# Kernel optimization log

Hardware: AMD Instinct MI355X
Metric: run time of the kernel (lower is better)

The kernel has to match this reference:

```python
import jax, jax.numpy as jnp
import numpy as np

BN_EPS = 1e-5
MAX_NODES = 35  # sigmoid()*30+5 floored -> in [5, 34], strict bound 35


def _bn_eval(x, gamma, beta, rm, rv):
    # BatchNorm1d in eval mode with running statistics
    return (x - rm) * (gamma / jnp.sqrt(rv + BN_EPS)) + beta


def setup_inputs() -> dict:
    key = jax.random.key(0)
    ks = jax.random.split(key, 32)
    B, LD, E, ND = 131072, 32, 64, 11

    def lin(k, fan_in, fan_out):
        k1, k2 = jax.random.split(k)
        lim = 1.0 / np.sqrt(fan_in)
        w = jax.random.uniform(k1, (fan_in, fan_out), jnp.float32, -lim, lim)
        b = jax.random.uniform(k2, (fan_out,), jnp.float32, -lim, lim)
        return w, b

    lin_w, lin_b = lin(ks[0], LD + 1, E)
    nn1_w, nn1_b = lin(ks[1], E, E)
    nn2_w, nn2_b = lin(ks[2], E, 1)
    nd1_w, nd1_b = lin(ks[3], E, E)
    nd2_w, nd2_b = lin(ks[4], E, ND)
    pd1_w, pd1_b = lin(ks[5], E, E)
    pd2_w, pd2_b = lin(ks[6], E, 3)

    def bn_params(k):
        k1, k2, k3, k4 = jax.random.split(k, 4)
        gamma = 1.0 + 0.1 * jax.random.normal(k1, (E,), jnp.float32)
        beta = 0.1 * jax.random.normal(k2, (E,), jnp.float32)
        rm = 0.1 * jax.random.normal(k3, (E,), jnp.float32)
        rv = jax.random.uniform(k4, (E,), jnp.float32, 0.5, 1.5)
        return gamma, beta, rm, rv

    nd_gamma, nd_beta, nd_rm, nd_rv = bn_params(ks[7])
    pd_gamma, pd_beta, pd_rm, pd_rv = bn_params(ks[8])

    return dict(
        z=jax.random.normal(ks[9], (B, LD), jnp.float32),
        target_property=jax.random.normal(ks[10], (B,), jnp.float32),
        batch_size=B,
        lin_w=lin_w, lin_b=lin_b,
        nn1_w=nn1_w, nn1_b=nn1_b, nn2_w=nn2_w, nn2_b=nn2_b,
        nd1_w=nd1_w, nd1_b=nd1_b, nd_gamma=nd_gamma, nd_beta=nd_beta,
        nd_rm=nd_rm, nd_rv=nd_rv, nd2_w=nd2_w, nd2_b=nd2_b,
        pd1_w=pd1_w, pd1_b=pd1_b, pd_gamma=pd_gamma, pd_beta=pd_beta,
        pd_rm=pd_rm, pd_rv=pd_rv, pd2_w=pd2_w, pd2_b=pd2_b,
        node_scale=jnp.float32(4.5), node_shift=jnp.float32(4.5),
        pos_scale=jnp.float32(5.0), pos_shift=jnp.float32(0.0),
    )


def reference(z, target_property, batch_size,
              lin_w, lin_b,
              nn1_w, nn1_b, nn2_w, nn2_b,
              nd1_w, nd1_b, nd_gamma, nd_beta, nd_rm, nd_rv, nd2_w, nd2_b,
              pd1_w, pd1_b, pd_gamma, pd_beta, pd_rm, pd_rv, pd2_w, pd2_b,
              node_scale, node_shift, pos_scale, pos_shift):
    tp = target_property.reshape(-1, 1)
    h = jnp.concatenate([z, tp], axis=1) @ lin_w + lin_b  # [B, E]

    nn_logit = jax.nn.relu(h @ nn1_w + nn1_b) @ nn2_w + nn2_b  # [B, 1]
    num_nodes = (jax.nn.sigmoid(nn_logit) * 30.0 + 5.0).astype(jnp.int32)[:, 0]  # [B]

    # Expanded rows per graph are identical copies of h[i], so decode once per
    # graph (BN in eval mode) and repeat -> same math as per-graph expand+MLP.
    nf = _bn_eval(jax.nn.relu(h @ nd1_w + nd1_b), nd_gamma, nd_beta, nd_rm, nd_rv) @ nd2_w + nd2_b
    nf = nf * node_scale + node_shift  # [B, 11]
    pos = _bn_eval(jax.nn.relu(h @ pd1_w + pd1_b), pd_gamma, pd_beta, pd_rm, pd_rv) @ pd2_w + pd2_b
    pos = pos * pos_scale + pos_shift  # [B, 3]

    total = batch_size * MAX_NODES  # static padded bound on ragged concat length
    node_features = jnp.repeat(nf, num_nodes, axis=0, total_repeat_length=total)
    positions = jnp.repeat(pos, num_nodes, axis=0, total_repeat_length=total)
    return node_features, positions, num_nodes
```

## Files before the change

### kernel.cpp

```cpp
#include <hip/hip_runtime.h>
#include <math.h>

typedef unsigned int u32;
typedef unsigned short u16;
typedef unsigned char u8;
typedef __attribute__((ext_vector_type(8))) short short8v;
typedef __attribute__((ext_vector_type(4))) float f32x4;

#define NDF 11
#define MAXN 35
#define RS 72

__device__ __forceinline__ u16 f2bf(float x) {
    u32 b = __float_as_uint(x);
    u32 r = (b + 0x7fffu + ((b >> 16) & 1u)) >> 16;
    return (u16)r;
}
__device__ __forceinline__ float bf2f(u16 h) {
    return __uint_as_float(((u32)h) << 16);
}
__device__ __forceinline__ void splitbf(float x, u16& hi, u16& lo) {
    hi = f2bf(x);
    lo = f2bf(x - bf2f(hi));
}

__global__ void k_prep(const float* __restrict__ lin_w,
                       const float* __restrict__ nn1_w, const float* __restrict__ nn2_w,
                       const float* __restrict__ nd1_w, const float* __restrict__ nd2_w,
                       const float* __restrict__ pd1_w, const float* __restrict__ pd2_w,
                       const float* __restrict__ nd_g, const float* __restrict__ nd_be,
                       const float* __restrict__ nd_rm, const float* __restrict__ nd_rv,
                       const float* __restrict__ pd_g, const float* __restrict__ pd_be,
                       const float* __restrict__ pd_rm, const float* __restrict__ pd_rv,
                       u16* __restrict__ lint, u16* __restrict__ w1t3,
                       u16* __restrict__ w2t3, float* __restrict__ bnc)
{
    const int t0 = blockIdx.x * 256 + threadIdx.x;
    if (t0 < 64) {
        const float sc = nd_g[t0] / sqrtf(nd_rv[t0] + 1e-5f);
        bnc[t0]       = sc;
        bnc[64 + t0]  = nd_be[t0] - nd_rm[t0] * sc;
        const float sp = pd_g[t0] / sqrtf(pd_rv[t0] + 1e-5f);
        bnc[128 + t0] = sp;
        bnc[192 + t0] = pd_be[t0] - pd_rm[t0] * sp;
    }
    for (int i = t0; i < 64*RS; i += 4096) {
        const int n = i / RS, k = i % RS;
        const float v = (k < 33) ? lin_w[k*64 + n] : 0.f;
        u16 h, l; splitbf(v, h, l);
        lint[i] = h; lint[64*RS + i] = l;
    }
    for (int b = 0; b < 3; b++) {
        const float* M = (b == 0) ? nn1_w : (b == 1) ? nd1_w : pd1_w;
        u16* dst = w1t3 + (size_t)b * 2 * 64 * RS;
        for (int i = t0; i < 64*RS; i += 4096) {
            const int o = i / RS, k = i % RS;
            const float v = (k < 64) ? M[k*64 + o] : 0.f;
            u16 h, l; splitbf(v, h, l);
            dst[i] = h; dst[64*RS + i] = l;
        }
        u16* d2 = w2t3 + (size_t)b * 2 * 16 * RS;
        for (int i = t0; i < 16*RS; i += 4096) {
            const int n = i / RS, k = i % RS;
            float v = 0.f;
            if (k < 64) {
                if (b == 0)      { if (n == 14)           v = nn2_w[k]; }
                else if (b == 1) { if (n < 11)            v = nd2_w[k*11 + n]; }
                else             { if (n >= 11 && n < 14) v = pd2_w[k*3 + (n-11)]; }
            }
            u16 h, l; splitbf(v, h, l);
            d2[i] = h; d2[16*RS + i] = l;
        }
    }
}

__global__ __launch_bounds__(256)
void k_mfma(const float* __restrict__ z, const float* __restrict__ tpr,
            const float* __restrict__ lin_b,
            const u16* __restrict__ lint, const u16* __restrict__ w1t3,
            const u16* __restrict__ w2t3,
            const float* __restrict__ nn1_b, const float* __restrict__ nd1_b,
            const float* __restrict__ pd1_b,
            const float* __restrict__ nn2_b, const float* __restrict__ nd2_b,
            const float* __restrict__ pd2_b,
            const float* __restrict__ bnc,
            const float* __restrict__ nsc, const float* __restrict__ nsh,
            const float* __restrict__ psc, const float* __restrict__ psh,
            float* __restrict__ nf_g, float* __restrict__ pos_g,
            int* __restrict__ nn_int, float* __restrict__ out_nn,
            u8* __restrict__ flag, int B)
{
    __shared__ __align__(16) u16 sXT[4][2*16*RS];
    __shared__ __align__(16) u16 sH[4][2*16*RS];

    const int t    = threadIdx.x;
    const int lane = t & 63;
    const int w    = t >> 6;
    u16* mX = sXT[w];
    u16* mH = sH[w];

    const int W = blockIdx.x * 4 + w;

    auto zeroXpad = [&]() {
        if (lane < 16) {
            #pragma unroll
            for (int pl = 0; pl < 2; pl++) {
                u16* base = mX + pl*16*RS;
                base[lane*RS + 33] = 0;
                u32* p = (u32*)(base + lane*RS + 34);
                #pragma unroll
                for (int q = 0; q < 15; q++) p[q] = 0;
            }
        }
    };

    auto gfrag = [&](const u16* base, int row0, int ks) -> short8v {
        const uint4 v = *(const uint4*)(base + (row0 + (lane & 15))*RS + ks*32 + ((lane >> 4) * 8));
        return __builtin_bit_cast(short8v, v);
    };
    short8v fLin[4][2], fW[3][4][2], fH2[3][2];
    #pragma unroll
    for (int nt = 0; nt < 4; nt++)
        #pragma unroll
        for (int ks = 0; ks < 2; ks++)
            fLin[nt][ks] = gfrag(lint, nt*16, ks);
    #pragma unroll
    for (int b = 0; b < 3; b++)
        #pragma unroll
        for (int nt = 0; nt < 4; nt++)
            #pragma unroll
            for (int ks = 0; ks < 2; ks++)
                fW[b][nt][ks] = gfrag(w1t3 + (size_t)b*2*64*RS, nt*16, ks);
    #pragma unroll
    for (int b = 0; b < 3; b++)
        #pragma unroll
        for (int ks = 0; ks < 2; ks++)
            fH2[b][ks] = gfrag(w2t3 + (size_t)b*2*16*RS, 0, ks);

    const int col = lane & 15;
    float bLin[4], bB1[3][4], bSc[2][4], bBi[2][4];
    #pragma unroll
    for (int nt = 0; nt < 4; nt++) {
        const int c = nt*16 + col;
        bLin[nt]    = lin_b[c];
        bB1[0][nt]  = nn1_b[c];
        bB1[1][nt]  = nd1_b[c];
        bB1[2][nt]  = pd1_b[c];
        bSc[0][nt]  = bnc[c];        bBi[0][nt] = bnc[64 + c];
        bSc[1][nt]  = bnc[128 + c];  bBi[1][nt] = bnc[192 + c];
    }
    const float epb = (col < 11) ? nd2_b[col] : (col < 14) ? pd2_b[col - 11] : 0.f;
    const float nn2b = nn2_b[0];
    const float a_ns = nsc[0], a_nh = nsh[0], a_ps = psc[0], a_ph = psh[0];

    auto ldfrag = [&](const u16* base, int ks) -> short8v {
        const uint4 v = *(const uint4*)(base + (lane & 15)*RS + ks*32 + ((lane >> 4) * 8));
        return __builtin_bit_cast(short8v, v);
    };

    #pragma unroll 1
    for (int c = 0; c < 2; c++) {
        const int gb = (W*2 + c) * 16;
        if (gb >= B) break;

        zeroXpad();

        {
            const float4* zb = (const float4*)(z + (size_t)gb * 32);
            const float4 v0 = zb[(lane >> 2)*8 + (lane & 3)*2];
            const float4 v1 = zb[(lane >> 2)*8 + (lane & 3)*2 + 1];
            const float xv[8] = {v0.x, v0.y, v0.z, v0.w, v1.x, v1.y, v1.z, v1.w};
            u32 pkh[4], pkl[4];
            #pragma unroll
            for (int q = 0; q < 4; q++) {
                u16 h0, l0, h1, l1;
                splitbf(xv[2*q], h0, l0);
                splitbf(xv[2*q+1], h1, l1);
                pkh[q] = (u32)h0 | ((u32)h1 << 16);
                pkl[q] = (u32)l0 | ((u32)l1 << 16);
            }
            *(uint4*)(mX + (lane >> 2)*RS + (lane & 3)*8) = *(uint4*)pkh;
            *(uint4*)(mX + 16*RS + (lane >> 2)*RS + (lane & 3)*8) = *(uint4*)pkl;
            if (lane < 16) {
                u16 h, l; splitbf(tpr[gb + lane], h, l);
                mX[lane*RS + 32] = h;
                mX[16*RS + lane*RS + 32] = l;
            }
        }

        const short8v a0h = ldfrag(mX, 0);
        const short8v a1h = ldfrag(mX, 1);
        const short8v a0l = ldfrag(mX + 16*RS, 0);
        const short8v a1l = ldfrag(mX + 16*RS, 1);
        #pragma unroll
        for (int nt = 0; nt < 4; nt++) {
            const short8v bl0 = gfrag(lint + 64*RS, nt*16, 0);
            const short8v bl1 = gfrag(lint + 64*RS, nt*16, 1);
            f32x4 acc = {0.f, 0.f, 0.f, 0.f};
            acc = __builtin_amdgcn_mfma_f32_16x16x32_bf16(a0h, fLin[nt][0], acc, 0, 0, 0);
            acc = __builtin_amdgcn_mfma_f32_16x16x32_bf16(a1h, fLin[nt][1], acc, 0, 0, 0);
            acc = __builtin_amdgcn_mfma_f32_16x16x32_bf16(a0h, bl0, acc, 0, 0, 0);
            acc = __builtin_amdgcn_mfma_f32_16x16x32_bf16(a1h, bl1, acc, 0, 0, 0);
            acc = __builtin_amdgcn_mfma_f32_16x16x32_bf16(a0l, fLin[nt][0], acc, 0, 0, 0);
            acc = __builtin_amdgcn_mfma_f32_16x16x32_bf16(a1l, fLin[nt][1], acc, 0, 0, 0);
            const float bias = bLin[nt];
            #pragma unroll
            for (int r = 0; r < 4; r++) {
                const int row = (lane >> 4)*4 + r;
                u16 hh, hl; splitbf(acc[r] + bias, hh, hl);
                mH[row*RS + nt*16 + col] = hh;
                mH[16*RS + row*RS + nt*16 + col] = hl;
            }
        }

        u16* mT = mX;
        const short8v h0h = ldfrag(mH, 0);
        const short8v h1h = ldfrag(mH, 1);
        f32x4 acc2 = {0.f, 0.f, 0.f, 0.f};

        {
            const short8v h0l = ldfrag(mH + 16*RS, 0);
            const short8v h1l = ldfrag(mH + 16*RS, 1);
            const u16* wlo = w1t3 + 64*RS;
            #pragma unroll
            for (int nt = 0; nt < 4; nt++) {
                const short8v wl0 = gfrag(wlo, nt*16, 0);
                const short8v wl1 = gfrag(wlo, nt*16, 1);
                f32x4 acc = {0.f, 0.f, 0.f, 0.f};
                acc = __builtin_amdgcn_mfma_f32_16x16x32_bf16(h0h, fW[0][nt][0], acc, 0, 0, 0);
                acc = __builtin_amdgcn_mfma_f32_16x16x32_bf16(h1h, fW[0][nt][1], acc, 0, 0, 0);
                acc = __builtin_amdgcn_mfma_f32_16x16x32_bf16(h0h, wl0, acc, 0, 0, 0);
                acc = __builtin_amdgcn_mfma_f32_16x16x32_bf16(h1h, wl1, acc, 0, 0, 0);
                acc = __builtin_amdgcn_mfma_f32_16x16x32_bf16(h0l, fW[0][nt][0], acc, 0, 0, 0);
                acc = __builtin_amdgcn_mfma_f32_16x16x32_bf16(h1l, fW[0][nt][1], acc, 0, 0, 0);
                const float bb = bB1[0][nt];
                #pragma unroll
                for (int r = 0; r < 4; r++) {
                    const int row = (lane >> 4)*4 + r;
                    float rv = acc[r] + bb;
                    rv = rv > 0.f ? rv : 0.f;
                    u16 th, tl; splitbf(rv, th, tl);
                    mT[row*RS + nt*16 + col] = th;
                    mT[16*RS + row*RS + nt*16 + col] = tl;
                }
            }
            const short8v t0h = ldfrag(mT, 0);
            const short8v t1h = ldfrag(mT, 1);
            const short8v t0l = ldfrag(mT + 16*RS, 0);
            const short8v t1l = ldfrag(mT + 16*RS, 1);
            const short8v g2l0 = gfrag(w2t3 + 16*RS, 0, 0);
            const short8v g2l1 = gfrag(w2t3 + 16*RS, 0, 1);
            acc2 = __builtin_amdgcn_mfma_f32_16x16x32_bf16(t0h, fH2[0][0], acc2, 0, 0, 0);
            acc2 = __builtin_amdgcn_mfma_f32_16x16x32_bf16(t1h, fH2[0][1], acc2, 0, 0, 0);
            acc2 = __builtin_amdgcn_mfma_f32_16x16x32_bf16(t0h, g2l0, acc2, 0, 0, 0);
            acc2 = __builtin_amdgcn_mfma_f32_16x16x32_bf16(t1h, g2l1, acc2, 0, 0, 0);
            acc2 = __builtin_amdgcn_mfma_f32_16x16x32_bf16(t0l, fH2[0][0], acc2, 0, 0, 0);
            acc2 = __builtin_amdgcn_mfma_f32_16x16x32_bf16(t1l, fH2[0][1], acc2, 0, 0, 0);
        }

        #pragma unroll
        for (int b = 1; b < 3; b++) {
            #pragma unroll
            for (int nt = 0; nt < 4; nt++) {
                f32x4 acc = {0.f, 0.f, 0.f, 0.f};
                acc = __builtin_amdgcn_mfma_f32_16x16x32_bf16(h0h, fW[b][nt][0], acc, 0, 0, 0);
                acc = __builtin_amdgcn_mfma_f32_16x16x32_bf16(h1h, fW[b][nt][1], acc, 0, 0, 0);
                const float bb = bB1[b][nt];
                const float sc = bSc[b-1][nt];
                const float bi = bBi[b-1][nt];
                #pragma unroll
                for (int r = 0; r < 4; r++) {
                    const int row = (lane >> 4)*4 + r;
                    float rv = acc[r] + bb;
                    rv = rv > 0.f ? rv : 0.f;
                    mT[row*RS + nt*16 + col] = f2bf(fmaf(rv, sc, bi));
                }
            }
            const short8v t0 = ldfrag(mT, 0);
            const short8v t1 = ldfrag(mT, 1);
            acc2 = __builtin_amdgcn_mfma_f32_16x16x32_bf16(t0, fH2[b][0], acc2, 0, 0, 0);
            acc2 = __builtin_amdgcn_mfma_f32_16x16x32_bf16(t1, fH2[b][1], acc2, 0, 0, 0);
        }

        #pragma unroll
        for (int r = 0; r < 4; r++) {
            const int g = gb + (lane >> 4)*4 + r;
            const float v = acc2[r];
            if (col < 11) {
                nf_g[(size_t)g*NDF + col] = fmaf(v + epb, a_ns, a_nh);
            } else if (col < 14) {
                pos_g[(size_t)g*3 + (col - 11)] = fmaf(v + epb, a_ps, a_ph);
            } else if (col == 14) {
                const float logit = v + nn2b;
                const float arg = fmaf(1.f / (1.f + expf(-logit)), 30.f, 5.f);
                const int n = (int)arg;
                nn_int[g] = n;
                out_nn[g] = (float)n;
                flag[g] = (fabsf(arg - rintf(arg)) < 0.03f) ? 1 : 0;
            }
        }
    }
    (void)B;
}

__global__ __launch_bounds__(256)
void k_fix(const float* __restrict__ z, const float* __restrict__ tpr,
           const float* __restrict__ lin_w, const float* __restrict__ lin_b,
           const float* __restrict__ nn1_w, const float* __restrict__ nn1_b,
           const float* __restrict__ nn2_w, const float* __restrict__ nn2_b,
           const u8* __restrict__ flag, int* __restrict__ nn_int,
           float* __restrict__ out_nn, int B)
{
    __shared__ __align__(16) double hb[4][64];
    const int lane = threadIdx.x & 63;
    const int w = threadIdx.x >> 6;
    const int W = (blockIdx.x * 256 + threadIdx.x) >> 6;
    const int gpw = B / 4096;
    const int g0 = W * gpw;
    const double b2 = (double)nn2_b[0];

    for (int i = 0; i < gpw; i++) {
        const int g = g0 + i;
        if (!flag[g]) continue;

        double h0 = (double)lin_b[lane], h1 = 0.0, h2 = 0.0, h3 = 0.0;
        for (int j = 0; j < 32; j += 4) {
            h0 = fma((double)z[(size_t)g*32 + j],     (double)lin_w[j*64 + lane],     h0);
            h1 = fma((double)z[(size_t)g*32 + j + 1], (double)lin_w[(j+1)*64 + lane], h1);
            h2 = fma((double)z[(size_t)g*32 + j + 2], (double)lin_w[(j+2)*64 + lane], h2);
            h3 = fma((double)z[(size_t)g*32 + j + 3], (double)lin_w[(j+3)*64 + lane], h3);
        }
        h0 = fma((double)tpr[g], (double)lin_w[32*64 + lane], h0);
        hb[w][lane] = (h0 + h1) + (h2 + h3);

        const double2* hp = (const double2*)hb[w];
        double a0 = (double)nn1_b[lane], a1 = 0.0, a2 = 0.0, a3 = 0.0;
        for (int m = 0; m < 16; m++) {
            const double2 p = hp[2*m];
            const double2 q = hp[2*m + 1];
            a0 = fma(p.x, (double)nn1_w[(4*m+0)*64 + lane], a0);
            a1 = fma(p.y, (double)nn1_w[(4*m+1)*64 + lane], a1);
            a2 = fma(q.x, (double)nn1_w[(4*m+2)*64 + lane], a2);
            a3 = fma(q.y, (double)nn1_w[(4*m+3)*64 + lane], a3);
        }
        const double a = (a0 + a1) + (a2 + a3);
        double v = (a > 0.0) ? a * (double)nn2_w[lane] : 0.0;
        for (int d = 32; d > 0; d >>= 1) v += __shfl_xor(v, d);
        const double logit = v + b2;

        if (lane == 0) {
            const double sg = 1.0 / (1.0 + exp(-logit));
            const int n = (int)(sg * 30.0 + 5.0);
            nn_int[g] = n;
            out_nn[g] = (float)n;
        }
    }
}

__global__ __launch_bounds__(256)
void k_scan1(const int* __restrict__ a, int* __restrict__ part, int* __restrict__ bsum)
{
    const int t = threadIdx.x;
    const int lane = t & 63;
    const int wid = t >> 6;
    const int g = blockIdx.x * 256 + t;
    int v = a[g];
    #pragma unroll
    for (int d = 1; d < 64; d <<= 1) {
        const int u = __shfl_up(v, d);
        if (lane >= d) v += u;
    }
    __shared__ int ws[4];
    if (lane == 63) ws[wid] = v;
    __syncthreads();
    int add = 0;
    #pragma unroll
    for (int q = 0; q < 3; q++) if (q < wid) add += ws[q];
    v += add;
    part[g] = v;
    if (t == 255) bsum[blockIdx.x] = v;
}

__global__ void k_scan2(const int* __restrict__ bsum, int* __restrict__ boff, int nb)
{
    const int t = threadIdx.x;
    const int lane = t & 63;
    const int wid = t >> 6;
    const int orig = bsum[t];
    int v = orig;
    #pragma unroll
    for (int d = 1; d < 64; d <<= 1) {
        const int u = __shfl_up(v, d);
        if (lane >= d) v += u;
    }
    __shared__ int ws[8];
    if (lane == 63) ws[wid] = v;
    __syncthreads();
    int add = 0;
    #pragma unroll
    for (int q = 0; q < 7; q++) if (q < wid) add += ws[q];
    v += add;
    boff[t] = v - orig;
    if (t == nb - 1) boff[nb] = v;
}

__global__ __launch_bounds__(256)
void k_expand(const int* __restrict__ part, const int* __restrict__ boff,
              const float* __restrict__ nf_g, const float* __restrict__ pos_g,
              float* __restrict__ out, int B, int T, int nb)
{
    __shared__ __align__(16) float s_nf[512*NDF];
    __shared__ __align__(16) float s_ps[512*3];
    const int t = threadIdx.x;
    const int r0 = blockIdx.x * 512 + 2*t;

    int blo = 0, bhi = nb - 1;
    while (blo < bhi) {
        const int m = (blo + bhi + 1) >> 1;
        if (boff[m] <= r0) blo = m; else bhi = m - 1;
    }
    const int bi = blo;
    const int lr = r0 - boff[bi];
    int lo = 0, hi2 = 256;
    while (lo < hi2) {
        const int m = (lo + hi2) >> 1;
        if (part[bi*256 + m] <= lr) lo = m + 1; else hi2 = m;
    }
    int i0 = bi*256 + lo;
    i0 = (i0 < B) ? i0 : B - 1;
    const int Ci0 = boff[i0 >> 8] + part[i0];
    const int i1 = ((r0 + 1) >= Ci0 && i0 < B - 1) ? i0 + 1 : i0;

    #pragma unroll
    for (int j = 0; j < NDF; j++) {
        s_nf[(2*t)*NDF + j]     = nf_g[(size_t)i0*NDF + j];
        s_nf[(2*t + 1)*NDF + j] = nf_g[(size_t)i1*NDF + j];
    }
    #pragma unroll
    for (int j = 0; j < 3; j++) {
        s_ps[(2*t)*3 + j]     = pos_g[(size_t)i0*3 + j];
        s_ps[(2*t + 1)*3 + j] = pos_g[(size_t)i1*3 + j];
    }
    __syncthreads();

    float4* onf = (float4*)(out + (size_t)blockIdx.x * 512 * NDF);
    const float4* snf = (const float4*)s_nf;
    #pragma unroll
    for (int q = 0; q < 6; q++) {
        const int idx = q*256 + t;
        if (idx < 512*NDF/4) onf[idx] = snf[idx];
    }
    float4* ops = (float4*)(out + (size_t)T*NDF + (size_t)blockIdx.x * 512 * 3);
    const float4* sps = (const float4*)s_ps;
    #pragma unroll
    for (int q = 0; q < 2; q++) {
        const int idx = q*256 + t;
        if (idx < 384) ops[idx] = sps[idx];
    }
}

extern "C" void kernel_launch(void* const* d_in, const int* in_sizes, int n_in,
                              void* d_out, int out_size, void* d_ws, size_t ws_size,
                              hipStream_t stream)
{
    const float* z     = (const float*)d_in[0];
    const float* tpr   = (const float*)d_in[1];
    const int    B     = in_sizes[1];
    const int    T     = B * MAXN;

    const float* lin_w = (const float*)d_in[3];
    const float* lin_b = (const float*)d_in[4];
    const float* nn1_w = (const float*)d_in[5];
    const float* nn1_b = (const float*)d_in[6];
    const float* nn2_w = (const float*)d_in[7];
    const float* nn2_b = (const float*)d_in[8];
    const float* nd1_w = (const float*)d_in[9];
    const float* nd1_b = (const float*)d_in[10];
    const float* nd_g  = (const float*)d_in[11];
    const float* nd_be = (const float*)d_in[12];
    const float* nd_rm = (const float*)d_in[13];
    const float* nd_rv = (const float*)d_in[14];
    const float* nd2_w = (const float*)d_in[15];
    const float* nd2_b = (const float*)d_in[16];
    const float* pd1_w = (const float*)d_in[17];
    const float* pd1_b = (const float*)d_in[18];
    const float* pd_g  = (const float*)d_in[19];
    const float* pd_be = (const float*)d_in[20];
    const float* pd_rm = (const float*)d_in[21];
    const float* pd_rv = (const float*)d_in[22];
    const float* pd2_w = (const float*)d_in[23];
    const float* pd2_b = (const float*)d_in[24];
    const float* nsc   = (const float*)d_in[25];
    const float* nsh   = (const float*)d_in[26];
    const float* psc   = (const float*)d_in[27];
    const float* psh   = (const float*)d_in[28];

    float* out = (float*)d_out;

    char* wsp = (char*)d_ws;
    size_t off = 0;
    auto take = [&](size_t bytes) { void* p = wsp + off; off = (off + bytes + 255) & ~(size_t)255; return p; };

    u16*   lint  = (u16*)take(2*64*RS*sizeof(u16));
    u16*   w1t3  = (u16*)take(3*2*64*RS*sizeof(u16));
    u16*   w2t3  = (u16*)take(3*2*16*RS*sizeof(u16));
    float* bnc   = (float*)take(256*sizeof(float));
    u8*    flag  = (u8*)take((size_t)B);
    float* nf_g  = (float*)take((size_t)B*NDF*sizeof(float));
    float* pos_g = (float*)take((size_t)B*3*sizeof(float));
    int*   nn_i  = (int*)take((size_t)B*sizeof(int));
    int*   part  = (int*)take((size_t)B*sizeof(int));
    int*   bsum  = (int*)take(4096*sizeof(int));
    int*   boff  = (int*)take(4096*sizeof(int));

    const int nb = B / 256;

    k_prep<<<16, 256, 0, stream>>>(lin_w, nn1_w, nn2_w, nd1_w, nd2_w, pd1_w, pd2_w,
                                   nd_g, nd_be, nd_rm, nd_rv,
                                   pd_g, pd_be, pd_rm, pd_rv,
                                   lint, w1t3, w2t3, bnc);

    k_mfma<<<B/128, 256, 0, stream>>>(z, tpr, lin_b, lint, w1t3, w2t3,
                                      nn1_b, nd1_b, pd1_b, nn2_b, nd2_b, pd2_b,
                                      bnc, nsc, nsh, psc, psh,
                                      nf_g, pos_g, nn_i, out + (size_t)T*14,
                                      flag, B);

    k_fix<<<1024, 256, 0, stream>>>(z, tpr, lin_w, lin_b, nn1_w, nn1_b, nn2_w, nn2_b,
                                    flag, nn_i, out + (size_t)T*14, B);

    k_scan1<<<nb, 256, 0, stream>>>(nn_i, part, bsum);
    k_scan2<<<1, nb, 0, stream>>>(bsum, boff, nb);

    k_expand<<<T/512, 256, 0, stream>>>(part, boff, nf_g, pos_g, out, B, T, nb);

    (void)n_in; (void)out_size; (void)ws_size;
}
```

Baseline: 141.6 us.

## Pack fix-up flags into per-wave bitmasks and cache block offsets in LDS

The MFMA kernel now ballots its near-integer flags into a 32-bit mask per wave instead of writing a byte per graph. The double-precision fix-up kernel iterates only over set bits, so it no longer scans every flag byte. Graphs whose sigmoid output saturates near 5 or 35 are resolved directly, which removes spurious flags at the clamp edges. The expand kernel also stages the block-offset table in shared memory for its binary search, at the cost of an extra sync and a shared-memory fill per block.

```diff
diff --git a/kernel.cpp b/kernel.cpp
--- a/kernel.cpp
+++ b/kernel.cpp
@@ -3,7 +3,6 @@
 
 typedef unsigned int u32;
 typedef unsigned short u16;
-typedef unsigned char u8;
 typedef __attribute__((ext_vector_type(8))) short short8v;
 typedef __attribute__((ext_vector_type(4))) float f32x4;
 
@@ -88,7 +87,7 @@
             const float* __restrict__ psc, const float* __restrict__ psh,
             float* __restrict__ nf_g, float* __restrict__ pos_g,
             int* __restrict__ nn_int, float* __restrict__ out_nn,
-            u8* __restrict__ flag, int B)
+            u32* __restrict__ fmask, int B)
 {
     __shared__ __align__(16) u16 sXT[4][2*16*RS];
     __shared__ __align__(16) u16 sH[4][2*16*RS];
@@ -157,6 +156,8 @@
         const uint4 v = *(const uint4*)(base + (lane & 15)*RS + ks*32 + ((lane >> 4) * 8));
         return __builtin_bit_cast(short8v, v);
     };
+
+    u32 wavebits = 0;
 
     #pragma unroll 1
     for (int c = 0; c < 2; c++) {
@@ -282,10 +283,12 @@
             acc2 = __builtin_amdgcn_mfma_f32_16x16x32_bf16(t1, fH2[b][1], acc2, 0, 0, 0);
         }
 
+        u32 chunkbits = 0;
         #pragma unroll
         for (int r = 0; r < 4; r++) {
             const int g = gb + (lane >> 4)*4 + r;
             const float v = acc2[r];
+            bool fl = false;
             if (col < 11) {
                 nf_g[(size_t)g*NDF + col] = fmaf(v + epb, a_ns, a_nh);
             } else if (col < 14) {
@@ -293,13 +296,29 @@
             } else if (col == 14) {
                 const float logit = v + nn2b;
                 const float arg = fmaf(1.f / (1.f + expf(-logit)), 30.f, 5.f);
-                const int n = (int)arg;
+                int n;
+                if (arg < 5.03f) {
+                    n = 5;
+                } else if (arg >= 34.97f) {
+                    if (logit >= 38.f)      n = 35;
+                    else { n = 34; fl = (logit > 37.f); }
+                } else {
+                    n = (int)arg;
+                    fl = fabsf(arg - rintf(arg)) < 0.03f;
+                }
                 nn_int[g] = n;
                 out_nn[g] = (float)n;
-                flag[g] = (fabsf(arg - rintf(arg)) < 0.03f) ? 1 : 0;
-            }
-        }
-    }
+            }
+            const unsigned long long m = __ballot(fl);
+            chunkbits |= (u32)(((m >> 14) & 1ull) << r)
+                       | (u32)(((m >> 30) & 1ull) << (4 + r))
+                       | (u32)(((m >> 46) & 1ull) << (8 + r))
+                       | (u32)(((m >> 62) & 1ull) << (12 + r));
+        }
+        wavebits |= chunkbits << (16 * c);
+    }
+
+    if (lane == 0) fmask[W] = wavebits;
     (void)B;
 }
 
@@ -308,20 +327,20 @@
            const float* __restrict__ lin_w, const float* __restrict__ lin_b,
            const float* __restrict__ nn1_w, const float* __restrict__ nn1_b,
            const float* __restrict__ nn2_w, const float* __restrict__ nn2_b,
-           const u8* __restrict__ flag, int* __restrict__ nn_int,
+           const u32* __restrict__ fmask, int* __restrict__ nn_int,
            float* __restrict__ out_nn, int B)
 {
     __shared__ __align__(16) double hb[4][64];
     const int lane = threadIdx.x & 63;
     const int w = threadIdx.x >> 6;
     const int W = (blockIdx.x * 256 + threadIdx.x) >> 6;
-    const int gpw = B / 4096;
-    const int g0 = W * gpw;
+    u32 mask = fmask[W];
     const double b2 = (double)nn2_b[0];
 
-    for (int i = 0; i < gpw; i++) {
-        const int g = g0 + i;
-        if (!flag[g]) continue;
+    while (mask) {
+        const int bpos = __ffs(mask) - 1;
+        mask &= mask - 1;
+        const int g = W * 32 + bpos;
 
         double h0 = (double)lin_b[lane], h1 = 0.0, h2 = 0.0, h3 = 0.0;
         for (int j = 0; j < 32; j += 4) {
@@ -355,6 +374,7 @@
             out_nn[g] = (float)n;
         }
     }
+    (void)B;
 }
 
 __global__ __launch_bounds__(256)
@@ -411,16 +431,20 @@
 {
     __shared__ __align__(16) float s_nf[512*NDF];
     __shared__ __align__(16) float s_ps[512*3];
+    __shared__ int s_boff[513];
     const int t = threadIdx.x;
+    for (int i = t; i <= nb; i += 256) s_boff[i] = boff[i];
+    __syncthreads();
+
     const int r0 = blockIdx.x * 512 + 2*t;
 
     int blo = 0, bhi = nb - 1;
     while (blo < bhi) {
         const int m = (blo + bhi + 1) >> 1;
-        if (boff[m] <= r0) blo = m; else bhi = m - 1;
+        if (s_boff[m] <= r0) blo = m; else bhi = m - 1;
     }
     const int bi = blo;
-    const int lr = r0 - boff[bi];
+    const int lr = r0 - s_boff[bi];
     int lo = 0, hi2 = 256;
     while (lo < hi2) {
         const int m = (lo + hi2) >> 1;
@@ -428,7 +452,7 @@
     }
     int i0 = bi*256 + lo;
     i0 = (i0 < B) ? i0 : B - 1;
-    const int Ci0 = boff[i0 >> 8] + part[i0];
+    const int Ci0 = s_boff[i0 >> 8] + part[i0];
     const int i1 = ((r0 + 1) >= Ci0 && i0 < B - 1) ? i0 + 1 : i0;
 
     #pragma unroll
@@ -505,7 +529,7 @@
     u16*   w1t3  = (u16*)take(3*2*64*RS*sizeof(u16));
     u16*   w2t3  = (u16*)take(3*2*16*RS*sizeof(u16));
     float* bnc   = (float*)take(256*sizeof(float));
-    u8*    flag  = (u8*)take((size_t)B);
+    u32*   fmask = (u32*)take((size_t)(B/32)*sizeof(u32));
     float* nf_g  = (float*)take((size_t)B*NDF*sizeof(float));
     float* pos_g = (float*)take((size_t)B*3*sizeof(float));
     int*   nn_i  = (int*)take((size_t)B*sizeof(int));
@@ -524,10 +548,10 @@
                                       nn1_b, nd1_b, pd1_b, nn2_b, nd2_b, pd2_b,
                                       bnc, nsc, nsh, psc, psh,
                                       nf_g, pos_g, nn_i, out + (size_t)T*14,
-                                      flag, B);
+                                      fmask, B);
 
     k_fix<<<1024, 256, 0, stream>>>(z, tpr, lin_w, lin_b, nn1_w, nn1_b, nn2_w, nn2_b,
-                                    flag, nn_i, out + (size_t)T*14, B);
+                                    fmask, nn_i, out + (size_t)T*14, B);
 
     k_scan1<<<nb, 256, 0, stream>>>(nn_i, part, bsum);
     k_scan2<<<1, nb, 0, stream>>>(bsum, boff, nb);
```

Measured after the change: 148.6 us. 1.05x slower.
